# Performance work log

Measured on AMD Instinct MI355X. Metric: run time of the kernel, lower is better.

## Reference

```python
import jax, jax.numpy as jnp
import numpy as np

D_MODEL = 1024
DIM_K = 1024
DIM_V = 1024
N_HEADS = 16
B, SX, SY = 4, 1024, 1024
NORM_FACT = float(1.0 / np.sqrt(D_MODEL))  # note: 1/sqrt(d_model), not head dim


def setup_inputs() -> dict:
    key = jax.random.key(0)
    ks = jax.random.split(key, 10)
    s = 0.02
    return {
        "x": jax.random.normal(ks[0], (B, SX, D_MODEL), jnp.float32),
        "y": jax.random.normal(ks[1], (B, SY, D_MODEL), jnp.float32),
        "Wq": jax.random.normal(ks[2], (DIM_K, D_MODEL), jnp.float32) * s,
        "bq": jax.random.normal(ks[3], (DIM_K,), jnp.float32) * s,
        "Wk": jax.random.normal(ks[4], (DIM_K, D_MODEL), jnp.float32) * s,
        "bk": jax.random.normal(ks[5], (DIM_K,), jnp.float32) * s,
        "Wv": jax.random.normal(ks[6], (DIM_V, D_MODEL), jnp.float32) * s,
        "bv": jax.random.normal(ks[7], (DIM_V,), jnp.float32) * s,
        "Wo": jax.random.normal(ks[8], (D_MODEL, DIM_V), jnp.float32) * s,
        "bo": jax.random.normal(ks[9], (D_MODEL,), jnp.float32) * s,
        "requires_mask": 1,
    }


def reference(x, y, Wq, bq, Wk, bk, Wv, bv, Wo, bo, requires_mask):
    b, sx, _ = x.shape
    sy = y.shape[1]
    dk_h = DIM_K // N_HEADS
    dv_h = DIM_V // N_HEADS
    # torch: q(x).reshape(-1, B, S, dk_h) -> raw row-major reshape puts heads first
    Q = (x @ Wq.T + bq).reshape(N_HEADS, b, sx, dk_h)
    K = (y @ Wk.T + bk).reshape(N_HEADS, b, sy, dk_h)
    V = (y @ Wv.T + bv).reshape(N_HEADS, b, sy, dv_h)

    score = jnp.einsum('hbsd,hbtd->hbst', Q, K) * NORM_FACT  # [H,B,Sx,Sy]
    # branch 1: softmax over query axis (-2), then L1-normalize rows
    attn = jax.nn.softmax(score, axis=-2)
    l1 = jnp.maximum(jnp.sum(jnp.abs(attn), axis=-1, keepdims=True), 1e-12)
    attn = attn / l1
    # branch 2: mean-threshold mask then row softmax
    score1 = score
    if requires_mask:
        thre = jnp.mean(score, axis=-1, keepdims=True)
        score1 = jnp.where(score - thre > 0, score, -jnp.inf)
    attn1 = jax.nn.softmax(score1, axis=-1)

    # torch: matmul(...).reshape(B, Sx, -1) -> raw reshape of [H,B,Sx,dv_h]
    out = jnp.einsum('hbst,hbtd->hbsd', attn, V).reshape(b, sx, -1)
    out1 = jnp.einsum('hbst,hbtd->hbsd', attn1, V).reshape(b, sx, -1)
    out = 0.5 * (out + out1)
    return out @ Wo.T + bo
```

## Files before the change

### kernel.cpp

```cpp
#include <hip/hip_runtime.h>
#include <hip/hip_bf16.h>
#include <stdint.h>

typedef float f32x4 __attribute__((ext_vector_type(4)));
typedef short bf16x8 __attribute__((ext_vector_type(8)));
typedef _Float16 f16x8 __attribute__((ext_vector_type(8)));

#define DEV static __device__ __forceinline__

DEV float bf2f(short u) {
  union { float f; unsigned i; } v;
  v.i = ((unsigned)(unsigned short)u) << 16;
  return v.f;
}
DEV short f2bf(float f) {
  union { float f; unsigned i; } v;
  v.f = f;
  unsigned lsb = (v.i >> 16) & 1u;
  v.i += 0x7fffu + lsb;
  return (short)(v.i >> 16);
}
DEV short f2h(float f) {
  union { _Float16 h; short s; } u;
  u.h = (_Float16)f;
  return u.s;
}

DEV void glds16(const void* g, void* l) {
  __builtin_amdgcn_global_load_lds(
      (const __attribute__((address_space(1))) void*)g,
      (__attribute__((address_space(3))) void*)l, 16, 0, 0);
}

__global__ __launch_bounds__(256) void k_convert(
    const float* __restrict__ x, const float* __restrict__ y,
    const float* __restrict__ wq, const float* __restrict__ wk,
    const float* __restrict__ wv, const float* __restrict__ wo,
    short* __restrict__ x16, short* __restrict__ y16,
    short* __restrict__ wq16, short* __restrict__ wk16,
    short* __restrict__ wv16, short* __restrict__ wohi) {
  const float* src; short* dst; int n, half;
  switch (blockIdx.y) {
    case 0: src = x;  dst = x16;  n = 4194304; half = 1; break;
    case 1: src = y;  dst = y16;  n = 4194304; half = 1; break;
    case 2: src = wq; dst = wq16; n = 1048576; half = 1; break;
    case 3: src = wk; dst = wk16; n = 1048576; half = 1; break;
    case 4: src = wv; dst = wv16; n = 1048576; half = 1; break;
    default: src = wo; dst = wohi; n = 1048576; half = 0; break;
  }
  int i4 = blockIdx.x * 256 + threadIdx.x;
  if (i4 * 4 >= n) return;
  float4 v = ((const float4*)src)[i4];
  short4 h;
  float* pv = (float*)&v;
  short* ph = (short*)&h;
#pragma unroll
  for (int e = 0; e < 4; ++e) ph[e] = half ? f2h(pv[e]) : f2bf(pv[e]);
  ((short4*)dst)[i4] = h;
}

DEV void gemm_block_map64(int wg, long& bRow, long& bCol) {
  int rlow = wg & 7, c = (wg >> 3) & 15, rhigh = wg >> 7;
  bRow = (long)(rhigh * 8 + rlow) * 128;
  bCol = (long)c * 64;
}

__global__ __launch_bounds__(256) void k_gemm_out(
    const short* __restrict__ A, const short* __restrict__ B,
    const float* __restrict__ bias, float* __restrict__ C, int M, int N, int K) {
  __shared__ __align__(16) short As[2][128 * 64];
  __shared__ __align__(16) short Bs[2][64 * 64];
  const int tid = threadIdx.x, lane = tid & 63;
  const int w = tid >> 6;
  const int lo = lane & 15, hi4 = lane >> 4;
  long bRow, bCol;
  gemm_block_map64(blockIdx.x, bRow, bCol);
  f32x4 acc[2][4] = {};
  const int nks = K >> 6;
  auto stage = [&](int buf, int ks) {
#pragma unroll
    for (int i = 0; i < 4; ++i) {
      int c = i * 256 + tid;
      int r = c >> 3;
      int wi = ((c & 7) * 16) ^ ((r & 7) << 4);
      glds16((const char*)A + (bRow + r) * (long)(K * 2) + ks * 128 + wi, (char*)As[buf] + c * 16);
    }
#pragma unroll
    for (int i = 0; i < 2; ++i) {
      int c = i * 256 + tid;
      int r = c >> 3;
      int wi = ((c & 7) * 16) ^ ((r & 7) << 4);
      glds16((const char*)B + (bCol + r) * (long)(K * 2) + ks * 128 + wi, (char*)Bs[buf] + c * 16);
    }
  };
  stage(0, 0);
  __syncthreads();
  int p = 0;
  for (int ks = 0; ks < nks; ++ks) {
    if (ks + 1 < nks) stage(p ^ 1, ks + 1);
#pragma unroll
    for (int kk = 0; kk < 2; ++kk) {
      bf16x8 af[2], bfr[4];
#pragma unroll
      for (int m = 0; m < 2; ++m) {
        int r = w * 32 + m * 16 + lo;
        af[m] = *(const bf16x8*)((const char*)As[p] + r * 128 + ((kk * 64 + hi4 * 16) ^ ((r & 7) << 4)));
      }
#pragma unroll
      for (int n = 0; n < 4; ++n) {
        int r = n * 16 + lo;
        bfr[n] = *(const bf16x8*)((const char*)Bs[p] + r * 128 + ((kk * 64 + hi4 * 16) ^ ((r & 7) << 4)));
      }
#pragma unroll
      for (int m = 0; m < 2; ++m)
#pragma unroll
        for (int n = 0; n < 4; ++n)
          acc[m][n] = __builtin_amdgcn_mfma_f32_16x16x32_bf16(af[m], bfr[n], acc[m][n], 0, 0, 0);
    }
    __syncthreads();
    p ^= 1;
  }
#pragma unroll
  for (int n = 0; n < 4; ++n) {
    long col = bCol + n * 16 + lo;
    float bv = bias[col];
#pragma unroll
    for (int m = 0; m < 2; ++m) {
      long row0 = bRow + w * 32 + m * 16 + hi4 * 4;
#pragma unroll
      for (int j = 0; j < 4; ++j)
        C[(row0 + j) * N + col] = acc[m][n][j] + bv;
    }
  }
}

template <int OUT_MODE>
__global__ __launch_bounds__(256) void k_gemm_f16(
    const short* __restrict__ A, const short* __restrict__ B,
    const float* __restrict__ bias, short* __restrict__ C, int M, int N, int K) {
  __shared__ __align__(16) short As[2][128 * 64];
  __shared__ __align__(16) short Bs[2][64 * 64];
  const int tid = threadIdx.x, lane = tid & 63;
  const int w = tid >> 6;
  const int lo = lane & 15, hi4 = lane >> 4;
  long bRow, bCol;
  gemm_block_map64(blockIdx.x, bRow, bCol);
  f32x4 acc[2][4] = {};
  const int nks = K >> 6;
  auto stage = [&](int buf, int ks) {
#pragma unroll
    for (int i = 0; i < 4; ++i) {
      int c = i * 256 + tid;
      int r = c >> 3;
      int wi = ((c & 7) * 16) ^ ((r & 7) << 4);
      glds16((const char*)A + (bRow + r) * (long)(K * 2) + ks * 128 + wi, (char*)As[buf] + c * 16);
    }
#pragma unroll
    for (int i = 0; i < 2; ++i) {
      int c = i * 256 + tid;
      int r = c >> 3;
      int wi = ((c & 7) * 16) ^ ((r & 7) << 4);
      glds16((const char*)B + (bCol + r) * (long)(K * 2) + ks * 128 + wi, (char*)Bs[buf] + c * 16);
    }
  };
  stage(0, 0);
  __syncthreads();
  int p = 0;
  for (int ks = 0; ks < nks; ++ks) {
    if (ks + 1 < nks) stage(p ^ 1, ks + 1);
#pragma unroll
    for (int kk = 0; kk < 2; ++kk) {
      f16x8 af[2], bfr[4];
#pragma unroll
      for (int m = 0; m < 2; ++m) {
        int r = w * 32 + m * 16 + lo;
        af[m] = *(const f16x8*)((const char*)As[p] + r * 128 + ((kk * 64 + hi4 * 16) ^ ((r & 7) << 4)));
      }
#pragma unroll
      for (int n = 0; n < 4; ++n) {
        int r = n * 16 + lo;
        bfr[n] = *(const f16x8*)((const char*)Bs[p] + r * 128 + ((kk * 64 + hi4 * 16) ^ ((r & 7) << 4)));
      }
#pragma unroll
      for (int m = 0; m < 2; ++m)
#pragma unroll
        for (int n = 0; n < 4; ++n)
          acc[m][n] = __builtin_amdgcn_mfma_f32_16x16x32_f16(af[m], bfr[n], acc[m][n], 0, 0, 0);
    }
    __syncthreads();
    p ^= 1;
  }
#pragma unroll
  for (int n = 0; n < 4; ++n) {
    long col = bCol + n * 16 + lo;
    float bv = bias[col];
#pragma unroll
    for (int m = 0; m < 2; ++m)
#pragma unroll
      for (int j = 0; j < 4; ++j) {
        long row = bRow + w * 32 + m * 16 + hi4 * 4 + j;
        float v = acc[m][n][j] + bv;
        C[row * N + col] = (OUT_MODE == 2) ? f2h(v) : f2bf(v);
      }
  }
}

__global__ __launch_bounds__(256) void k_mu(
    const short* __restrict__ K16, const short* __restrict__ Q16,
    float* __restrict__ Thr) {
  __shared__ float tmp[32][64];
  __shared__ float ksum[64];
  const int g = blockIdx.x >> 2, q = blockIdx.x & 3;
  const int tid = threadIdx.x;
  const int d8 = tid & 7, tq = tid >> 3;
  const short* kp = K16 + (long)g * 65536;
  float acc[8] = {};
  for (int t = tq; t < 1024; t += 32) {
    f16x8 a = *(const f16x8*)(kp + t * 64 + d8 * 8);
#pragma unroll
    for (int e = 0; e < 8; ++e) acc[e] += (float)a[e];
  }
#pragma unroll
  for (int e = 0; e < 8; ++e) tmp[tq][d8 * 8 + e] = acc[e];
  __syncthreads();
  if (tid < 64) {
    float s = 0.f;
#pragma unroll
    for (int qq = 0; qq < 32; ++qq) s += tmp[qq][tid];
    ksum[tid] = s;
  }
  __syncthreads();
  const float c = 0.03125f / 1024.f;
  const int s = q * 256 + tid;
  const short* qp = Q16 + (long)g * 65536 + s * 64;
  float dot = 0.f;
#pragma unroll
  for (int d0 = 0; d0 < 64; d0 += 8) {
    f16x8 a = *(const f16x8*)(qp + d0);
#pragma unroll
    for (int e = 0; e < 8; ++e) dot += (float)a[e] * ksum[d0 + e];
  }
  Thr[g * 1024 + s] = dot * c;
}

__global__ __launch_bounds__(256) void k_passA_fuse(
    const short* __restrict__ Q16, const short* __restrict__ K16,
    const short* __restrict__ Vb, short* __restrict__ Vt,
    short* __restrict__ rlbf) {
  __shared__ __align__(16) short Ks[64 * 64];
  __shared__ __align__(16) short Qs[2][64 * 64];
  __shared__ __align__(16) short T[64][80];
  __shared__ float rls[64];
  const int wg = blockIdx.x;
  const int g = (wg & 7) | ((wg >> 7) << 3);
  const int tb = (wg >> 3) & 15;
  const int tid = threadIdx.x, lane = tid & 63;
  const int w = tid >> 6;
  const int lo = lane & 15, hi4 = lane >> 4;
  const long gbase = (long)g * 131072;
  const float CEXP = 0.045136860026163146f;

  const short* vsrc = Vb + (long)g * 65536 + (long)tb * 64 * 64;
  bf16x8 vreg[2];
#pragma unroll
  for (int i = 0; i < 2; ++i) {
    int c = i * 256 + tid;
    vreg[i] = *(const bf16x8*)(vsrc + (c >> 3) * 64 + (c & 7) * 8);
  }

  auto stageQ = [&](int buf, int sb) {
#pragma unroll
    for (int i = 0; i < 2; ++i) {
      int c = i * 256 + tid;
      int r = c >> 3;
      int wi = ((c & 7) * 16) ^ ((r & 7) << 4);
      glds16((const char*)Q16 + gbase + (long)(sb * 64 + r) * 128 + wi, (char*)Qs[buf] + c * 16);
    }
  };
#pragma unroll
  for (int i = 0; i < 2; ++i) {
    int c = i * 256 + tid;
    int r = c >> 3;
    int wi = ((c & 7) * 16) ^ ((r & 7) << 4);
    glds16((const char*)K16 + gbase + (long)(tb * 64 + r) * 128 + wi, (char*)Ks + c * 16);
  }
  stageQ(0, 0);
  __syncthreads();
  f16x8 kf[2];
#pragma unroll
  for (int kk = 0; kk < 2; ++kk) {
    int r = w * 16 + lo;
    kf[kk] = *(const f16x8*)((const char*)Ks + r * 128 + ((kk * 64 + hi4 * 16) ^ ((r & 7) << 4)));
  }
  float Lacc[4] = {};
  int p = 0;
  for (int sb = 0; sb < 16; ++sb) {
    if (sb < 15) stageQ(p ^ 1, sb + 1);
    f32x4 s[4] = {};
#pragma unroll
    for (int kk = 0; kk < 2; ++kk) {
#pragma unroll
      for (int n = 0; n < 4; ++n) {
        int r = n * 16 + lo;
        f16x8 qf = *(const f16x8*)((const char*)Qs[p] + r * 128 +
                                   ((kk * 64 + hi4 * 16) ^ ((r & 7) << 4)));
        __builtin_amdgcn_s_setprio(1);
        s[n] = __builtin_amdgcn_mfma_f32_16x16x32_f16(kf[kk], qf, s[n], 0, 0, 0);
        __builtin_amdgcn_s_setprio(0);
      }
    }
#pragma unroll
    for (int n = 0; n < 4; ++n)
#pragma unroll
      for (int j = 0; j < 4; ++j)
        Lacc[j] += __builtin_amdgcn_exp2f(s[n][j] * CEXP);
    __syncthreads();
    p ^= 1;
  }
#pragma unroll
  for (int j = 0; j < 4; ++j) {
    float v = Lacc[j];
    v += __shfl_xor(v, 1);
    v += __shfl_xor(v, 2);
    v += __shfl_xor(v, 4);
    v += __shfl_xor(v, 8);
    if (lo == 0) {
      float rv = 1.0f / v;
      int idx = w * 16 + hi4 * 4 + j;
      rls[idx] = rv;
      rlbf[g * 1024 + tb * 64 + idx] = f2bf(rv);
    }
  }
  __syncthreads();
#pragma unroll
  for (int i = 0; i < 2; ++i) {
    int c = i * 256 + tid;
    int t = c >> 3, dc = (c & 7) * 8;
    float rv = rls[t];
#pragma unroll
    for (int e = 0; e < 8; ++e) T[dc + e][t] = f2bf(bf2f(vreg[i][e]) * rv);
  }
  __syncthreads();
  short* dst = Vt + (long)g * 65536 + tb * 64;
#pragma unroll
  for (int i = 0; i < 2; ++i) {
    int c = i * 256 + tid;
    int d = c >> 3, tc = (c & 7) * 8;
    bf16x8 o = *(const bf16x8*)(&T[d][tc]);
    *(bf16x8*)(dst + (long)d * 1024 + tc) = o;
  }
}

__global__ __launch_bounds__(256, 4) void k_passB(
    const short* __restrict__ Q16, const short* __restrict__ K16,
    const short* __restrict__ Vt, const short* __restrict__ rlbf,
    const float* __restrict__ Thr, short* __restrict__ Pre,
    const int* __restrict__ rmask) {
  __shared__ __align__(16) short Ks[2][64 * 64];
  __shared__ __align__(16) short Vs[2][64 * 64];
  __shared__ __align__(16) short Ps[64 * 64];
  const int wg = blockIdx.x;
  const int g = (wg & 7) | ((wg >> 7) << 3);
  const int rb = (wg >> 3) & 15;
  const int tid = threadIdx.x, lane = tid & 63;
  const int w = tid >> 6;
  const int lo = lane & 15, hi4 = lane >> 4;
  const long gbase = (long)g * 131072;
  const bool use_mask = (*rmask != 0);
  const int srow = w * 16 + lo;

  auto stage = [&](int buf, int tb2) {
#pragma unroll
    for (int i = 0; i < 2; ++i) {
      int c = i * 256 + tid;
      int r = c >> 3;
      int wi = ((c & 7) * 16) ^ ((r & 7) << 4);
      glds16((const char*)K16 + gbase + (long)(tb2 * 64 + r) * 128 + wi, (char*)Ks[buf] + c * 16);
      glds16((const char*)Vt + gbase + (long)r * 2048 + tb2 * 128 + wi, (char*)Vs[buf] + c * 16);
    }
  };

  f16x8 qf[2];
  {
    const char* qr = (const char*)Q16 + gbase + (long)(rb * 64 + srow) * 128;
#pragma unroll
    for (int kk = 0; kk < 2; ++kk)
      qf[kk] = *(const f16x8*)(qr + kk * 64 + hi4 * 16);
  }
  const float thre32 = use_mask ? Thr[g * 1024 + rb * 64 + srow] * 32.0f : -3.4e38f;
  const float CEXP = 0.045136860026163146f;
  f32x4 o1[4] = {}, o2[4] = {};
  f32x4 o1R = {}, o2Z = {};

  stage(0, 0);
  __syncthreads();
  int p = 0;
  for (int tb = 0; tb < 16; ++tb) {
    if (tb < 15) stage(p ^ 1, tb + 1);
    f32x4 s[4] = {};
#pragma unroll
    for (int kk = 0; kk < 2; ++kk) {
#pragma unroll
      for (int n = 0; n < 4; ++n) {
        int r = n * 16 + lo;
        f16x8 kf = *(const f16x8*)((const char*)Ks[p] + r * 128 +
                                   ((kk * 64 + hi4 * 16) ^ ((r & 7) << 4)));
        __builtin_amdgcn_s_setprio(1);
        s[n] = __builtin_amdgcn_mfma_f32_16x16x32_f16(kf, qf[kk], s[n], 0, 0, 0);
        __builtin_amdgcn_s_setprio(0);
      }
    }
    unsigned p2w0[4], p2w1[4];
#pragma unroll
    for (int n = 0; n < 4; ++n) {
      float ev[4], p2v[4];
#pragma unroll
      for (int j = 0; j < 4; ++j) {
        float sraw = s[n][j];
        float e = __builtin_amdgcn_exp2f(sraw * CEXP);
        ev[j] = e;
        p2v[j] = (sraw > thre32) ? e : 0.f;
      }
      unsigned u10, u11, u20, u21;
      asm("v_cvt_pk_bf16_f32 %0, %1, %2" : "=v"(u10) : "v"(ev[0]), "v"(ev[1]));
      asm("v_cvt_pk_bf16_f32 %0, %1, %2" : "=v"(u11) : "v"(ev[2]), "v"(ev[3]));
      asm("v_cvt_pk_bf16_f32 %0, %1, %2" : "=v"(u20) : "v"(p2v[0]), "v"(p2v[1]));
      asm("v_cvt_pk_bf16_f32 %0, %1, %2" : "=v"(u21) : "v"(p2v[2]), "v"(p2v[3]));
      p2w0[n] = u20;
      p2w1[n] = u21;
      int colb = n * 32 + hi4 * 8;
      int boff = srow * 128 + (colb ^ ((srow & 7) << 4));
      uint2 w1; w1.x = u10; w1.y = u11;
      *(uint2*)((char*)Ps + boff) = w1;
    }
    bf16x8 vbreg[2][4], rlfr[2];
#pragma unroll
    for (int kk = 0; kk < 2; ++kk) {
      int poff = srow * 128 + ((kk * 64 + hi4 * 16) ^ ((srow & 7) << 4));
      bf16x8 pa1 = *(const bf16x8*)((const char*)Ps + poff);
      rlfr[kk] = *(const bf16x8*)(rlbf + g * 1024 + tb * 64 + kk * 32 + hi4 * 8);
      __builtin_amdgcn_s_setprio(1);
      o1R = __builtin_amdgcn_mfma_f32_16x16x32_bf16(pa1, rlfr[kk], o1R, 0, 0, 0);
      __builtin_amdgcn_s_setprio(0);
#pragma unroll
      for (int n = 0; n < 4; ++n) {
        int d = n * 16 + lo;
        vbreg[kk][n] = *(const bf16x8*)((const char*)Vs[p] + d * 128 +
                                        ((kk * 64 + hi4 * 16) ^ ((d & 7) << 4)));
        __builtin_amdgcn_s_setprio(1);
        o1[n] = __builtin_amdgcn_mfma_f32_16x16x32_bf16(pa1, vbreg[kk][n], o1[n], 0, 0, 0);
        __builtin_amdgcn_s_setprio(0);
      }
    }
#pragma unroll
    for (int n = 0; n < 4; ++n) {
      int colb = n * 32 + hi4 * 8;
      int boff = srow * 128 + (colb ^ ((srow & 7) << 4));
      uint2 w2; w2.x = p2w0[n]; w2.y = p2w1[n];
      *(uint2*)((char*)Ps + boff) = w2;
    }
#pragma unroll
    for (int kk = 0; kk < 2; ++kk) {
      int poff = srow * 128 + ((kk * 64 + hi4 * 16) ^ ((srow & 7) << 4));
      bf16x8 pa2 = *(const bf16x8*)((const char*)Ps + poff);
      __builtin_amdgcn_s_setprio(1);
      o2Z = __builtin_amdgcn_mfma_f32_16x16x32_bf16(pa2, rlfr[kk], o2Z, 0, 0, 0);
#pragma unroll
      for (int n = 0; n < 4; ++n)
        o2[n] = __builtin_amdgcn_mfma_f32_16x16x32_bf16(pa2, vbreg[kk][n], o2[n], 0, 0, 0);
      __builtin_amdgcn_s_setprio(0);
    }
    __syncthreads();
    p ^= 1;
  }
#pragma unroll
  for (int j = 0; j < 4; ++j) {
    float rr = fmaxf(o1R[j], 1e-12f);
    float zz = fmaxf(o2Z[j], 1e-30f);
    float rinv = 0.5f / rr;
    float zinv = 0.5f / zz;
    int rl_ = w * 16 + hi4 * 4 + j;
#pragma unroll
    for (int n = 0; n < 4; ++n) {
      float val = o1[n][j] * rinv + o2[n][j] * zinv;
      Pre[(long)g * 65536 + (long)(rb * 64 + rl_) * 64 + n * 16 + lo] = f2bf(val);
    }
  }
}

extern "C" void kernel_launch(void* const* d_in, const int* in_sizes, int n_in,
                              void* d_out, int out_size, void* d_ws, size_t ws_size,
                              hipStream_t stream) {
  const float* x  = (const float*)d_in[0];
  const float* y  = (const float*)d_in[1];
  const float* Wq = (const float*)d_in[2];
  const float* bq = (const float*)d_in[3];
  const float* Wk = (const float*)d_in[4];
  const float* bk = (const float*)d_in[5];
  const float* Wv = (const float*)d_in[6];
  const float* bv = (const float*)d_in[7];
  const float* Wo = (const float*)d_in[8];
  const float* bo = (const float*)d_in[9];
  const int* rm   = (const int*)d_in[10];
  float* out = (float*)d_out;

  char* ws = (char*)d_ws;
  size_t off = 0;
  auto alloc = [&](size_t bytes) {
    char* p = ws + off;
    off += (bytes + 255) & ~(size_t)255;
    return p;
  };
  short* x16  = (short*)alloc(4194304 * 2);
  short* y16  = (short*)alloc(4194304 * 2);
  short* wq16 = (short*)alloc(1048576 * 2);
  short* wk16 = (short*)alloc(1048576 * 2);
  short* wv16 = (short*)alloc(1048576 * 2);
  short* wohi = (short*)alloc(1048576 * 2);
  short* Q16  = (short*)alloc(4194304 * 2);
  short* K16  = (short*)alloc(4194304 * 2);
  short* Vb   = (short*)alloc(4194304 * 2);
  short* VtB  = (short*)alloc(4194304 * 2);
  short* pre  = (short*)alloc(4194304 * 2);
  short* rlbf = (short*)alloc(65536 * 2);
  float* Thr  = (float*)alloc(65536 * 4);
  if (off > ws_size) return;

  k_convert<<<dim3(4096, 6), 256, 0, stream>>>(x, y, Wq, Wk, Wv, Wo,
                                               x16, y16, wq16, wk16, wv16, wohi);

  k_gemm_f16<2><<<512, 256, 0, stream>>>(x16, wq16, bq, Q16, 4096, 1024, 1024);
  k_gemm_f16<2><<<512, 256, 0, stream>>>(y16, wk16, bk, K16, 4096, 1024, 1024);
  k_gemm_f16<0><<<512, 256, 0, stream>>>(y16, wv16, bv, Vb, 4096, 1024, 1024);
  k_mu<<<256, 256, 0, stream>>>(K16, Q16, Thr);
  k_passA_fuse<<<1024, 256, 0, stream>>>(Q16, K16, Vb, VtB, rlbf);
  k_passB<<<1024, 256, 0, stream>>>(Q16, K16, VtB, rlbf, Thr, pre, rm);
  k_gemm_out<<<512, 256, 0, stream>>>(pre, wohi, bo, out, 4096, 1024, 1024);
}
```

Before: 156.0 us.

## Process 128 query rows per block in passB to reuse K/V tiles

Each wave now handles two 16-row query sub-tiles, so a passB block covers 128 query rows instead of 64 and the grid halves to 512 blocks. Every K and V tile staged into LDS and every V fragment loaded into registers now feeds twice as many MFMAs, which halves global-to-LDS traffic for K and V. The cost is more accumulator registers, a larger P buffer in LDS, launch bounds lowered to 2 blocks per CU, and fewer blocks to spread across CUs.

```diff
diff --git a/kernel.cpp b/kernel.cpp
--- a/kernel.cpp
+++ b/kernel.cpp
@@ -351,23 +351,23 @@
   }
 }
 
-__global__ __launch_bounds__(256, 4) void k_passB(
+__global__ __launch_bounds__(256, 2) void k_passB(
     const short* __restrict__ Q16, const short* __restrict__ K16,
     const short* __restrict__ Vt, const short* __restrict__ rlbf,
     const float* __restrict__ Thr, short* __restrict__ Pre,
     const int* __restrict__ rmask) {
   __shared__ __align__(16) short Ks[2][64 * 64];
   __shared__ __align__(16) short Vs[2][64 * 64];
-  __shared__ __align__(16) short Ps[64 * 64];
+  __shared__ __align__(16) short Ps[128 * 64];
   const int wg = blockIdx.x;
-  const int g = (wg & 7) | ((wg >> 7) << 3);
-  const int rb = (wg >> 3) & 15;
+  const int g = (wg & 7) | ((wg >> 6) << 3);
+  const int rb = (wg >> 3) & 7;
   const int tid = threadIdx.x, lane = tid & 63;
   const int w = tid >> 6;
   const int lo = lane & 15, hi4 = lane >> 4;
   const long gbase = (long)g * 131072;
   const bool use_mask = (*rmask != 0);
-  const int srow = w * 16 + lo;
+  const float CEXP = 0.045136860026163146f;
 
   auto stage = [&](int buf, int tb2) {
 #pragma unroll
@@ -380,24 +380,27 @@
     }
   };
 
-  f16x8 qf[2];
-  {
-    const char* qr = (const char*)Q16 + gbase + (long)(rb * 64 + srow) * 128;
+  f16x8 qf[2][2];
+  float thre32[2];
+#pragma unroll
+  for (int u = 0; u < 2; ++u) {
+    int srow = w * 32 + u * 16 + lo;
+    const char* qr = (const char*)Q16 + gbase + (long)(rb * 128 + srow) * 128;
 #pragma unroll
     for (int kk = 0; kk < 2; ++kk)
-      qf[kk] = *(const f16x8*)(qr + kk * 64 + hi4 * 16);
-  }
-  const float thre32 = use_mask ? Thr[g * 1024 + rb * 64 + srow] * 32.0f : -3.4e38f;
-  const float CEXP = 0.045136860026163146f;
-  f32x4 o1[4] = {}, o2[4] = {};
-  f32x4 o1R = {}, o2Z = {};
+      qf[u][kk] = *(const f16x8*)(qr + kk * 64 + hi4 * 16);
+    thre32[u] = use_mask ? Thr[g * 1024 + rb * 128 + srow] * 32.0f : -3.4e38f;
+  }
+
+  f32x4 o1[2][4] = {}, o2[2][4] = {};
+  f32x4 o1R[2] = {}, o2Z[2] = {};
 
   stage(0, 0);
   __syncthreads();
   int p = 0;
   for (int tb = 0; tb < 16; ++tb) {
     if (tb < 15) stage(p ^ 1, tb + 1);
-    f32x4 s[4] = {};
+    f32x4 s0[4] = {}, s1[4] = {};
 #pragma unroll
     for (int kk = 0; kk < 2; ++kk) {
 #pragma unroll
@@ -406,86 +409,106 @@
         f16x8 kf = *(const f16x8*)((const char*)Ks[p] + r * 128 +
                                    ((kk * 64 + hi4 * 16) ^ ((r & 7) << 4)));
         __builtin_amdgcn_s_setprio(1);
-        s[n] = __builtin_amdgcn_mfma_f32_16x16x32_f16(kf, qf[kk], s[n], 0, 0, 0);
+        s0[n] = __builtin_amdgcn_mfma_f32_16x16x32_f16(kf, qf[0][kk], s0[n], 0, 0, 0);
+        s1[n] = __builtin_amdgcn_mfma_f32_16x16x32_f16(kf, qf[1][kk], s1[n], 0, 0, 0);
         __builtin_amdgcn_s_setprio(0);
       }
     }
-    unsigned p2w0[4], p2w1[4];
-#pragma unroll
-    for (int n = 0; n < 4; ++n) {
-      float ev[4], p2v[4];
-#pragma unroll
-      for (int j = 0; j < 4; ++j) {
-        float sraw = s[n][j];
-        float e = __builtin_amdgcn_exp2f(sraw * CEXP);
-        ev[j] = e;
-        p2v[j] = (sraw > thre32) ? e : 0.f;
-      }
-      unsigned u10, u11, u20, u21;
-      asm("v_cvt_pk_bf16_f32 %0, %1, %2" : "=v"(u10) : "v"(ev[0]), "v"(ev[1]));
-      asm("v_cvt_pk_bf16_f32 %0, %1, %2" : "=v"(u11) : "v"(ev[2]), "v"(ev[3]));
-      asm("v_cvt_pk_bf16_f32 %0, %1, %2" : "=v"(u20) : "v"(p2v[0]), "v"(p2v[1]));
-      asm("v_cvt_pk_bf16_f32 %0, %1, %2" : "=v"(u21) : "v"(p2v[2]), "v"(p2v[3]));
-      p2w0[n] = u20;
-      p2w1[n] = u21;
-      int colb = n * 32 + hi4 * 8;
-      int boff = srow * 128 + (colb ^ ((srow & 7) << 4));
-      uint2 w1; w1.x = u10; w1.y = u11;
-      *(uint2*)((char*)Ps + boff) = w1;
+    unsigned p2w0[2][4], p2w1[2][4];
+#pragma unroll
+    for (int u = 0; u < 2; ++u) {
+      int prow = w * 32 + u * 16 + lo;
+#pragma unroll
+      for (int n = 0; n < 4; ++n) {
+        f32x4 sv = u ? s1[n] : s0[n];
+        float ev[4], p2v[4];
+#pragma unroll
+        for (int j = 0; j < 4; ++j) {
+          float sraw = sv[j];
+          float e = __builtin_amdgcn_exp2f(sraw * CEXP);
+          ev[j] = e;
+          p2v[j] = (sraw > thre32[u]) ? e : 0.f;
+        }
+        unsigned u10, u11, u20, u21;
+        asm("v_cvt_pk_bf16_f32 %0, %1, %2" : "=v"(u10) : "v"(ev[0]), "v"(ev[1]));
+        asm("v_cvt_pk_bf16_f32 %0, %1, %2" : "=v"(u11) : "v"(ev[2]), "v"(ev[3]));
+        asm("v_cvt_pk_bf16_f32 %0, %1, %2" : "=v"(u20) : "v"(p2v[0]), "v"(p2v[1]));
+        asm("v_cvt_pk_bf16_f32 %0, %1, %2" : "=v"(u21) : "v"(p2v[2]), "v"(p2v[3]));
+        p2w0[u][n] = u20;
+        p2w1[u][n] = u21;
+        int colb = n * 32 + hi4 * 8;
+        int boff = prow * 128 + (colb ^ ((prow & 7) << 4));
+        uint2 w1; w1.x = u10; w1.y = u11;
+        *(uint2*)((char*)Ps + boff) = w1;
+      }
     }
     bf16x8 vbreg[2][4], rlfr[2];
 #pragma unroll
     for (int kk = 0; kk < 2; ++kk) {
-      int poff = srow * 128 + ((kk * 64 + hi4 * 16) ^ ((srow & 7) << 4));
-      bf16x8 pa1 = *(const bf16x8*)((const char*)Ps + poff);
       rlfr[kk] = *(const bf16x8*)(rlbf + g * 1024 + tb * 64 + kk * 32 + hi4 * 8);
-      __builtin_amdgcn_s_setprio(1);
-      o1R = __builtin_amdgcn_mfma_f32_16x16x32_bf16(pa1, rlfr[kk], o1R, 0, 0, 0);
-      __builtin_amdgcn_s_setprio(0);
 #pragma unroll
       for (int n = 0; n < 4; ++n) {
         int d = n * 16 + lo;
         vbreg[kk][n] = *(const bf16x8*)((const char*)Vs[p] + d * 128 +
                                         ((kk * 64 + hi4 * 16) ^ ((d & 7) << 4)));
+      }
+#pragma unroll
+      for (int u = 0; u < 2; ++u) {
+        int prow = w * 32 + u * 16 + lo;
+        int poff = prow * 128 + ((kk * 64 + hi4 * 16) ^ ((prow & 7) << 4));
+        bf16x8 pa1 = *(const bf16x8*)((const char*)Ps + poff);
         __builtin_amdgcn_s_setprio(1);
-        o1[n] = __builtin_amdgcn_mfma_f32_16x16x32_bf16(pa1, vbreg[kk][n], o1[n], 0, 0, 0);
+        o1R[u] = __builtin_amdgcn_mfma_f32_16x16x32_bf16(pa1, rlfr[kk], o1R[u], 0, 0, 0);
+#pragma unroll
+        for (int n = 0; n < 4; ++n)
+          o1[u][n] = __builtin_amdgcn_mfma_f32_16x16x32_bf16(pa1, vbreg[kk][n], o1[u][n], 0, 0, 0);
         __builtin_amdgcn_s_setprio(0);
       }
     }
 #pragma unroll
-    for (int n = 0; n < 4; ++n) {
-      int colb = n * 32 + hi4 * 8;
-      int boff = srow * 128 + (colb ^ ((srow & 7) << 4));
-      uint2 w2; w2.x = p2w0[n]; w2.y = p2w1[n];
-      *(uint2*)((char*)Ps + boff) = w2;
+    for (int u = 0; u < 2; ++u) {
+      int prow = w * 32 + u * 16 + lo;
+#pragma unroll
+      for (int n = 0; n < 4; ++n) {
+        int colb = n * 32 + hi4 * 8;
+        int boff = prow * 128 + (colb ^ ((prow & 7) << 4));
+        uint2 w2; w2.x = p2w0[u][n]; w2.y = p2w1[u][n];
+        *(uint2*)((char*)Ps + boff) = w2;
+      }
     }
 #pragma unroll
     for (int kk = 0; kk < 2; ++kk) {
-      int poff = srow * 128 + ((kk * 64 + hi4 * 16) ^ ((srow & 7) << 4));
-      bf16x8 pa2 = *(const bf16x8*)((const char*)Ps + poff);
-      __builtin_amdgcn_s_setprio(1);
-      o2Z = __builtin_amdgcn_mfma_f32_16x16x32_bf16(pa2, rlfr[kk], o2Z, 0, 0, 0);
-#pragma unroll
-      for (int n = 0; n < 4; ++n)
-        o2[n] = __builtin_amdgcn_mfma_f32_16x16x32_bf16(pa2, vbreg[kk][n], o2[n], 0, 0, 0);
-      __builtin_amdgcn_s_setprio(0);
+#pragma unroll
+      for (int u = 0; u < 2; ++u) {
+        int prow = w * 32 + u * 16 + lo;
+        int poff = prow * 128 + ((kk * 64 + hi4 * 16) ^ ((prow & 7) << 4));
+        bf16x8 pa2 = *(const bf16x8*)((const char*)Ps + poff);
+        __builtin_amdgcn_s_setprio(1);
+        o2Z[u] = __builtin_amdgcn_mfma_f32_16x16x32_bf16(pa2, rlfr[kk], o2Z[u], 0, 0, 0);
+#pragma unroll
+        for (int n = 0; n < 4; ++n)
+          o2[u][n] = __builtin_amdgcn_mfma_f32_16x16x32_bf16(pa2, vbreg[kk][n], o2[u][n], 0, 0, 0);
+        __builtin_amdgcn_s_setprio(0);
+      }
     }
     __syncthreads();
     p ^= 1;
   }
 #pragma unroll
-  for (int j = 0; j < 4; ++j) {
-    float rr = fmaxf(o1R[j], 1e-12f);
-    float zz = fmaxf(o2Z[j], 1e-30f);
-    float rinv = 0.5f / rr;
-    float zinv = 0.5f / zz;
-    int rl_ = w * 16 + hi4 * 4 + j;
-#pragma unroll
-    for (int n = 0; n < 4; ++n) {
-      float val = o1[n][j] * rinv + o2[n][j] * zinv;
-      Pre[(long)g * 65536 + (long)(rb * 64 + rl_) * 64 + n * 16 + lo] = f2bf(val);
-    }
-  }
+  for (int u = 0; u < 2; ++u)
+#pragma unroll
+    for (int j = 0; j < 4; ++j) {
+      float rr = fmaxf(o1R[u][j], 1e-12f);
+      float zz = fmaxf(o2Z[u][j], 1e-30f);
+      float rinv = 0.5f / rr;
+      float zinv = 0.5f / zz;
+      int row = rb * 128 + w * 32 + u * 16 + hi4 * 4 + j;
+#pragma unroll
+      for (int n = 0; n < 4; ++n) {
+        float val = o1[u][n][j] * rinv + o2[u][n][j] * zinv;
+        Pre[(long)g * 65536 + (long)row * 64 + n * 16 + lo] = f2bf(val);
+      }
+    }
 }
 
 extern "C" void kernel_launch(void* const* d_in, const int* in_sizes, int n_in,
@@ -534,6 +557,6 @@
   k_gemm_f16<0><<<512, 256, 0, stream>>>(y16, wv16, bv, Vb, 4096, 1024, 1024);
   k_mu<<<256, 256, 0, stream>>>(K16, Q16, Thr);
   k_passA_fuse<<<1024, 256, 0, stream>>>(Q16, K16, Vb, VtB, rlbf);
-  k_passB<<<1024, 256, 0, stream>>>(Q16, K16, VtB, rlbf, Thr, pre, rm);
+  k_passB<<<512, 256, 0, stream>>>(Q16, K16, VtB, rlbf, Thr, pre, rm);
   k_gemm_out<<<512, 256, 0, stream>>>(pre, wohi, bo, out, 4096, 1024, 1024);
 }
```

After: 156.5 us. About the same (+0.3%).
